# Kernel optimization log

Hardware: AMD Instinct MI355X
Metric: run time of the kernel (lower is better)

## Reference

```python
import jax, jax.numpy as jnp
import numpy as np

SINK_SIZE = 1          # sink frames kept at front of cache
LOCAL_ATTN_SIZE = 6    # attention window in frames


def _rope_angles(max_len, dim, theta=10000.0):
    inv = 1.0 / (theta ** (np.arange(0, dim, 2, dtype=np.float64) / dim))
    return np.outer(np.arange(max_len, dtype=np.float64), inv)  # [max_len, dim//2]


def _freqs_table(head_dim):
    # matches torch.cat([rope_params(1024, d-4*(d//6)), rope_params(1024, 2*(d//6)) x2], dim=1)
    d = head_dim
    return np.concatenate([
        _rope_angles(1024, d - 4 * (d // 6)),
        _rope_angles(1024, 2 * (d // 6)),
        _rope_angles(1024, 2 * (d // 6)),
    ], axis=1).astype(np.float32)  # [1024, d//2]


def _apply_rope(x, f, h, w, start_frame, freqs):
    # x: [B, S, N, D] with S == f*h*w; complex RoPE expressed as cos/sin rotation
    B, S, N, D = x.shape
    c = D // 2
    s0, s1 = c - 2 * (c // 3), c // 3
    ang = jnp.concatenate([
        jnp.broadcast_to(freqs[start_frame:start_frame + f, :s0][:, None, None, :], (f, h, w, s0)),
        jnp.broadcast_to(freqs[:h, s0:s0 + s1][None, :, None, :], (f, h, w, s1)),
        jnp.broadcast_to(freqs[:w, s0 + s1:][None, None, :, :], (f, h, w, s1)),
    ], axis=-1).reshape(S, 1, c)
    cos, sin = jnp.cos(ang)[None], jnp.sin(ang)[None]  # [1, S, 1, c]
    xr = x.reshape(B, S, N, c, 2)
    x0, x1 = xr[..., 0], xr[..., 1]
    out = jnp.stack([x0 * cos - x1 * sin, x0 * sin + x1 * cos], axis=-1)
    return out.reshape(B, S, N, D)


def setup_inputs() -> dict:
    key = jax.random.key(0)
    ks = jax.random.split(key, 5)
    B, S, N, D = 1, 1920, 12, 128
    CACHE = 6720
    return {
        "q": jax.random.normal(ks[0], (B, S, N, D), dtype=jnp.float32),
        "k": jax.random.normal(ks[1], (B, S, N, D), dtype=jnp.float32),
        "v": jax.random.normal(ks[2], (B, S, N, D), dtype=jnp.float32),
        "cache_k": jax.random.normal(ks[3], (B, CACHE, N, D), dtype=jnp.float32),
        "cache_v": jax.random.normal(ks[4], (B, CACHE, N, D), dtype=jnp.float32),
        "f": 2, "h": 24, "w": 40,
        "current_start": 5760, "global_end": 5760, "local_end": 5760,
    }


def reference(q, k, v, cache_k, cache_v, f, h, w, current_start, global_end, local_end):
    D = q.shape[-1]
    freqs = jnp.asarray(_freqs_table(D))
    frame_seqlen = h * w
    start_frame = current_start // frame_seqlen

    rq = _apply_rope(q, f, h, w, start_frame, freqs)
    rk = _apply_rope(k, f, h, w, start_frame, freqs)

    sink = SINK_SIZE * frame_seqlen
    max_att = LOCAL_ATTN_SIZE * frame_seqlen
    kv_size = cache_k.shape[1]
    n_new = q.shape[1]
    current_end = current_start + n_new

    # streaming KV cache with sink tokens + eviction/roll (indices are static ints,
    # matching torch's .item()-driven control flow)
    if current_end > global_end and n_new + local_end > kv_size:
        ev = n_new + local_end - kv_size
        roll = local_end - ev - sink
        cache_k = cache_k.at[:, sink:sink + roll].set(cache_k[:, sink + ev:sink + ev + roll])
        cache_v = cache_v.at[:, sink:sink + roll].set(cache_v[:, sink + ev:sink + ev + roll])
        new_local_end = local_end + current_end - global_end - ev
    else:
        new_local_end = local_end + current_end - global_end
    local_start = new_local_end - n_new
    cache_k = cache_k.at[:, local_start:new_local_end].set(rk)
    cache_v = cache_v.at[:, local_start:new_local_end].set(v)

    kv_start = max(0, new_local_end - max_att)
    kk = cache_k[:, kv_start:new_local_end]  # [B, W, N, D]
    vv = cache_v[:, kv_start:new_local_end]

    scale = 1.0 / jnp.sqrt(jnp.float32(D))
    scores = jnp.einsum('bqnd,bknd->bnqk', rq, kk) * scale
    attn = jax.nn.softmax(scores, axis=-1)
    out = jnp.einsum('bnqk,bknd->bqnd', attn, vv)
    return out
```

## Files before the change

### kernel.cpp

```cpp
#include <hip/hip_runtime.h>
#include <hip/hip_bf16.h>
#include <math.h>

typedef __attribute__((ext_vector_type(8))) short short8;
typedef __attribute__((ext_vector_type(4))) float f32x4;
typedef unsigned int u32;
typedef unsigned short u16;

#define NH 12
#define SQ 1920
#define SK 5760
#define DH 128
#define QTILE 32
#define NQT (SQ / QTILE)
#define QCH (NQT / 4)

#define OFF_CT 0
#define OFF_ST (OFF_CT + SQ * 64 * 4)
#define OFF_QB (OFF_ST + SQ * 64 * 4)
#define OFF_KB (OFF_QB + NH * SQ * DH * 2)
#define OFF_VT (OFF_KB + NH * SK * DH * 2)
#define OFF_PO (OFF_VT + NH * SK * DH * 2)

__device__ __forceinline__ u16 f2bf(float f) {
  u32 x = __float_as_uint(f);
  x += 0x7fffu + ((x >> 16) & 1u);
  return (u16)(x >> 16);
}

__device__ __forceinline__ f32x4 ntload4(const float* p) {
  return __builtin_nontemporal_load((const f32x4*)p);
}
__device__ __forceinline__ void ntstore4(float* p, f32x4 v) {
  __builtin_nontemporal_store(v, (f32x4*)p);
}

__global__ void k_table(float* __restrict__ ct, float* __restrict__ st) {
  int idx = blockIdx.x * 256 + threadIdx.x;
  if (idx >= SQ * 64) return;
  int s = idx >> 6, j = idx & 63;
  int fi = s / 960, rem = s % 960, hi = rem / 40, wi = rem % 40;
  const float L2_10000 = 13.287712379549449f;
  float ang;
  if (j < 22)      ang = (float)(6 + fi) * exp2f(-L2_10000 * (2.0f * j) / 44.0f);
  else if (j < 43) ang = (float)hi * exp2f(-L2_10000 * (2.0f * (j - 22)) / 42.0f);
  else             ang = (float)wi * exp2f(-L2_10000 * (2.0f * (j - 43)) / 42.0f);
  ct[idx] = cosf(ang);
  st[idx] = sinf(ang);
}

__global__ void k_prep(const float* __restrict__ q, const float* __restrict__ k,
                       const float* __restrict__ cache_k,
                       const float* __restrict__ ct, const float* __restrict__ st,
                       u16* __restrict__ Qb, u16* __restrict__ Kb) {
  const int NQth = NH * SQ * 32;
  const int NKN  = NH * SQ * 32;
  int idx = blockIdx.x * 256 + threadIdx.x;
  if (idx < NQth) {
    int c = idx & 31; int sn = idx >> 5; int n = sn % NH; int s = sn / NH;
    float4 x = *(const float4*)(q + ((size_t)s * NH + n) * DH + c * 4);
    float c0 = ct[s * 64 + 2 * c], s0 = st[s * 64 + 2 * c];
    float c1 = ct[s * 64 + 2 * c + 1], s1 = st[s * 64 + 2 * c + 1];
    const float QSC = (float)(1.4426950408889634 / 11.313708498984760390);
    ushort4 w;
    w.x = f2bf((x.x * c0 - x.y * s0) * QSC);
    w.y = f2bf((x.x * s0 + x.y * c0) * QSC);
    w.z = f2bf((x.z * c1 - x.w * s1) * QSC);
    w.w = f2bf((x.z * s1 + x.w * c1) * QSC);
    *(ushort4*)(Qb + ((size_t)n * SQ + s) * DH + c * 4) = w;
  } else if (idx < NQth + NKN) {
    int t = idx - NQth;
    int c = t & 31; int sn = t >> 5; int n = sn % NH; int s = sn / NH;
    float4 x = *(const float4*)(k + ((size_t)s * NH + n) * DH + c * 4);
    float c0 = ct[s * 64 + 2 * c], s0 = st[s * 64 + 2 * c];
    float c1 = ct[s * 64 + 2 * c + 1], s1 = st[s * 64 + 2 * c + 1];
    ushort4 w;
    w.x = f2bf(x.x * c0 - x.y * s0);
    w.y = f2bf(x.x * s0 + x.y * c0);
    w.z = f2bf(x.z * c1 - x.w * s1);
    w.w = f2bf(x.z * s1 + x.w * c1);
    *(ushort4*)(Kb + ((size_t)n * SK + 3840 + s) * DH + c * 4) = w;
  } else {
    int t = idx - NQth - NKN;
    int c = t & 31; int sn = t >> 5; int n = sn % NH; int p = sn / NH;
    float4 x = *(const float4*)(cache_k + ((size_t)(1920 + p) * NH + n) * DH + c * 4);
    ushort4 w; w.x = f2bf(x.x); w.y = f2bf(x.y); w.z = f2bf(x.z); w.w = f2bf(x.w);
    *(ushort4*)(Kb + ((size_t)n * SK + p) * DH + c * 4) = w;
  }
}

__global__ void k_vt(const float* __restrict__ v, const float* __restrict__ cache_v,
                     u16* __restrict__ Vt) {
  __shared__ float tile[64][65];
  int b = blockIdx.x;
  int n = b / 180; int bh = b % 180; int pb = bh >> 1; int dhalf = bh & 1;
  int p0 = pb * 64, d0 = dhalf * 64;
  int t = threadIdx.x;
#pragma unroll
  for (int it = 0; it < 16; ++it) {
    int lin = t + it * 256;
    int r = lin >> 6, c = lin & 63;
    int p = p0 + r;
    float val = (p < 3840)
      ? cache_v[((size_t)(1920 + p) * NH + n) * DH + d0 + c]
      : v[((size_t)(p - 3840) * NH + n) * DH + d0 + c];
    tile[r][c] = val;
  }
  __syncthreads();
#pragma unroll
  for (int it = 0; it < 16; ++it) {
    int lin = t + it * 256;
    int dr = lin >> 6, pc = lin & 63;
    Vt[((size_t)n * DH + d0 + dr) * SK + p0 + pc] = f2bf(tile[pc][dr]);
  }
}

#define KE (32 * 128)
#define VE (128 * 32)

template <int NS>
__global__ __launch_bounds__(256, 3) void k_attn(
    const u16* __restrict__ Qb, const u16* __restrict__ Kb, const u16* __restrict__ Vt,
    float* __restrict__ PO, float* __restrict__ Pm, float* __restrict__ Ps) {
  const int KPB = SK / NS;
  const int ITERS = KPB / 32;
  __shared__ u16 Klds[3 * KE];
  __shared__ u16 Vlds[3 * VE];

  const int nwg = NH * QCH * NS;
  int bid = blockIdx.x;
  int widx = (bid & 7) * (nwg >> 3) + (bid >> 3);
  int n = widx / (QCH * NS);
  int j2 = widx % (QCH * NS);
  int sp = j2 / QCH;
  int qtb = j2 % QCH;

  int tid = threadIdx.x;
  int w = tid >> 6;
  int l = tid & 63;
  int col = l & 15, g = l >> 4;
  int qt = qtb * 4 + w;
  int q0 = qt * QTILE;
  int kb0 = sp * KPB;

  const u16* kgh = Kb + (size_t)n * SK * DH;
  const u16* vgh = Vt + (size_t)n * DH * SK;

  auto stage = [&](int b, int kb) {
    u16* kl = Klds + b * KE;
    u16* vl = Vlds + b * VE;
#pragma unroll
    for (int i = 0; i < 2; ++i) {
      int cb = (i * 4 + w) * 64;
      {
        int T = cb + l; int r = T >> 4; int c = (T & 15) ^ (r & 7);
        __builtin_amdgcn_global_load_lds(
            (const __attribute__((address_space(1))) void*)(kgh + ((size_t)(kb + r)) * DH + (c << 3)),
            (__attribute__((address_space(3))) void*)(kl + cb * 8), 16, 0, 0);
      }
      {
        int T = cb + l; int d = T >> 2; int c = (T & 3) ^ (d & 3);
        __builtin_amdgcn_global_load_lds(
            (const __attribute__((address_space(1))) void*)(vgh + (size_t)d * SK + kb + (c << 3)),
            (__attribute__((address_space(3))) void*)(vl + cb * 8), 16, 0, 0);
      }
    }
  };

  short8 aq[2][4];
#pragma unroll
  for (int u = 0; u < 2; ++u) {
    const u16* qr = Qb + ((size_t)n * SQ + q0 + u * 16 + col) * DH + g * 8;
#pragma unroll
    for (int ks = 0; ks < 4; ++ks)
      aq[u][ks] = __builtin_nontemporal_load((const short8*)(qr + ks * 32));
  }

  f32x4 o[2][8];
#pragma unroll
  for (int u = 0; u < 2; ++u)
#pragma unroll
    for (int dt = 0; dt < 8; ++dt) o[u][dt] = (f32x4){0.f, 0.f, 0.f, 0.f};
  float m[2] = {-1e30f, -1e30f}, ssum[2] = {0.f, 0.f};

  stage(0, kb0);
  stage(1, kb0 + 32);

  int cur = 0;
  const int xK = col & 7;
  const int vch = (g ^ (col & 3)) << 3;
  for (int t = 0; t < ITERS; ++t) {
    int kb = kb0 + t * 32;
    int b2 = cur + 2; if (b2 >= 3) b2 -= 3;
    if (t + 2 < ITERS) {
      stage(b2, kb + 64);
      asm volatile("s_waitcnt vmcnt(8)" ::: "memory");
    } else if (t + 1 < ITERS) {
      asm volatile("s_waitcnt vmcnt(4)" ::: "memory");
    } else {
      asm volatile("s_waitcnt vmcnt(0)" ::: "memory");
    }
    __builtin_amdgcn_s_barrier();
    __builtin_amdgcn_sched_barrier(0);

    const u16* Kl = Klds + cur * KE;
    const u16* Vl = Vlds + cur * VE;

    f32x4 s0[2], s1[2];
#pragma unroll
    for (int u = 0; u < 2; ++u) { s0[u] = (f32x4){0,0,0,0}; s1[u] = (f32x4){0,0,0,0}; }
#pragma unroll
    for (int ks = 0; ks < 4; ++ks) {
      int ch = (((g + (ks << 2)) ^ xK) << 3);
      short8 ak0 = *(const short8*)(Kl + col * DH + ch);
      short8 ak1 = *(const short8*)(Kl + (col + 16) * DH + ch);
      s0[0] = __builtin_amdgcn_mfma_f32_16x16x32_bf16(ak0, aq[0][ks], s0[0], 0, 0, 0);
      s0[1] = __builtin_amdgcn_mfma_f32_16x16x32_bf16(ak0, aq[1][ks], s0[1], 0, 0, 0);
      s1[0] = __builtin_amdgcn_mfma_f32_16x16x32_bf16(ak1, aq[0][ks], s1[0], 0, 0, 0);
      s1[1] = __builtin_amdgcn_mfma_f32_16x16x32_bf16(ak1, aq[1][ks], s1[1], 0, 0, 0);
    }
    u32 pw[2][4];
#pragma unroll
    for (int u = 0; u < 2; ++u) {
      float bm = fmaxf(fmaxf(fmaxf(s0[u][0], s0[u][1]), fmaxf(s0[u][2], s0[u][3])),
                       fmaxf(fmaxf(s1[u][0], s1[u][1]), fmaxf(s1[u][2], s1[u][3])));
      bm = fmaxf(bm, __shfl_xor(bm, 16));
      bm = fmaxf(bm, __shfl_xor(bm, 32));
      if (!__all(bm <= m[u] + 8.0f)) {
        float mn = fmaxf(m[u], bm);
        float cr = exp2f(m[u] - mn);
        ssum[u] *= cr;
#pragma unroll
        for (int dt = 0; dt < 8; ++dt) o[u][dt] *= cr;
        m[u] = mn;
      }
      float p[8];
      float bs = 0.f;
#pragma unroll
      for (int r = 0; r < 4; ++r) { p[r] = exp2f(s0[u][r] - m[u]); bs += p[r]; }
#pragma unroll
      for (int r = 0; r < 4; ++r) { p[4 + r] = exp2f(s1[u][r] - m[u]); bs += p[4 + r]; }
      bs += __shfl_xor(bs, 16);
      bs += __shfl_xor(bs, 32);
      ssum[u] += bs;
      u32 w0 = (u32)f2bf(p[0]) | ((u32)f2bf(p[1]) << 16);
      u32 w1 = (u32)f2bf(p[2]) | ((u32)f2bf(p[3]) << 16);
      u32 w2 = (u32)f2bf(p[4]) | ((u32)f2bf(p[5]) << 16);
      u32 w3 = (u32)f2bf(p[6]) | ((u32)f2bf(p[7]) << 16);
      int src0 = col + ((g & 1) << 5);
      int src1 = src0 + 16;
      u32 a0 = (u32)__shfl((int)w0, src0), a1 = (u32)__shfl((int)w1, src0);
      u32 a2 = (u32)__shfl((int)w0, src1), a3 = (u32)__shfl((int)w1, src1);
      u32 b0 = (u32)__shfl((int)w2, src0), b1 = (u32)__shfl((int)w3, src0);
      u32 b2v = (u32)__shfl((int)w2, src1), b3 = (u32)__shfl((int)w3, src1);
      bool hi = (g >= 2);
      pw[u][0] = hi ? b0 : a0; pw[u][1] = hi ? b1 : a1;
      pw[u][2] = hi ? b2v : a2; pw[u][3] = hi ? b3 : a3;
    }
#pragma unroll
    for (int dt = 0; dt < 8; ++dt) {
      short8 av = *(const short8*)(Vl + (dt * 16 + col) * 32 + vch);
      union { u32 w[4]; short8 v; } pu0, pu1;
#pragma unroll
      for (int i = 0; i < 4; ++i) { pu0.w[i] = pw[0][i]; pu1.w[i] = pw[1][i]; }
      o[0][dt] = __builtin_amdgcn_mfma_f32_16x16x32_bf16(av, pu0.v, o[0][dt], 0, 0, 0);
      o[1][dt] = __builtin_amdgcn_mfma_f32_16x16x32_bf16(av, pu1.v, o[1][dt], 0, 0, 0);
    }
    __builtin_amdgcn_sched_barrier(0);
    __builtin_amdgcn_s_barrier();
    cur = cur + 1 == 3 ? 0 : cur + 1;
  }

  int pb = (n * NQT + qt) * NS + sp;
  float* po = PO + (size_t)pb * QTILE * DH;
#pragma unroll
  for (int u = 0; u < 2; ++u) {
#pragma unroll
    for (int dt = 0; dt < 8; ++dt)
      ntstore4(po + ((size_t)(u * 16 + col)) * DH + dt * 16 + g * 4, o[u][dt]);
    if (g == 0) {
      Pm[pb * QTILE + u * 16 + col] = m[u];
      Ps[pb * QTILE + u * 16 + col] = ssum[u];
    }
  }
}

template <int NS>
__global__ void k_merge(const float* __restrict__ PO, const float* __restrict__ Pm,
                        const float* __restrict__ Ps, float* __restrict__ out) {
  int idx = blockIdx.x * 256 + threadIdx.x;
  if (idx >= NH * SQ * 32) return;
  int c = idx & 31; int rest = idx >> 5; int qh = rest % SQ; int n = rest / SQ;
  int qt = qh >> 5, row = qh & 31;
  int bb = (n * NQT + qt) * NS;
  float mm[NS];
  float M = -1e30f;
#pragma unroll
  for (int s = 0; s < NS; ++s) { mm[s] = Pm[(bb + s) * 32 + row]; M = fmaxf(M, mm[s]); }
  float wgt[NS];
  float denom = 0.f;
#pragma unroll
  for (int s = 0; s < NS; ++s) {
    wgt[s] = exp2f(mm[s] - M);
    denom += Ps[(bb + s) * 32 + row] * wgt[s];
  }
  float inv = 1.0f / denom;
  f32x4 r = {0.f, 0.f, 0.f, 0.f};
#pragma unroll
  for (int s = 0; s < NS; ++s) {
    f32x4 p = ntload4(PO + ((size_t)(bb + s) * 32 + row) * DH + c * 4);
    r += p * wgt[s];
  }
  r *= inv;
  ntstore4(out + ((size_t)qh * NH + n) * DH + c * 4, r);
}

template <int NS>
static bool do_launch(void* const* d_in, void* d_out, void* d_ws, size_t ws_size,
                      hipStream_t stream) {
  const size_t nblk = (size_t)NH * NQT * NS;
  const size_t off_pm = OFF_PO + nblk * QTILE * DH * 4;
  const size_t off_ps = off_pm + nblk * QTILE * 4;
  const size_t need = off_ps + nblk * QTILE * 4;
  if (ws_size < need) return false;
  const float* q  = (const float*)d_in[0];
  const float* k  = (const float*)d_in[1];
  const float* v  = (const float*)d_in[2];
  const float* ck = (const float*)d_in[3];
  const float* cv = (const float*)d_in[4];
  char* ws = (char*)d_ws;
  float* ct = (float*)(ws + OFF_CT);
  float* st = (float*)(ws + OFF_ST);
  u16* Qb = (u16*)(ws + OFF_QB);
  u16* Kb = (u16*)(ws + OFF_KB);
  u16* Vt = (u16*)(ws + OFF_VT);
  float* PO = (float*)(ws + OFF_PO);
  float* Pm = (float*)(ws + off_pm);
  float* Ps = (float*)(ws + off_ps);

  k_table<<<(SQ * 64 + 255) / 256, 256, 0, stream>>>(ct, st);
  k_prep<<<(NH * SQ * 32 * 2 + NH * 3840 * 32 + 255) / 256, 256, 0, stream>>>(
      q, k, ck, ct, st, Qb, Kb);
  k_vt<<<NH * 90 * 2, 256, 0, stream>>>(v, cv, Vt);
  k_attn<NS><<<NH * QCH * NS, 256, 0, stream>>>(Qb, Kb, Vt, PO, Pm, Ps);
  k_merge<NS><<<(NH * SQ * 32 + 255) / 256, 256, 0, stream>>>(PO, Pm, Ps, (float*)d_out);
  return true;
}

extern "C" void kernel_launch(void* const* d_in, const int* in_sizes, int n_in,
                              void* d_out, int out_size, void* d_ws, size_t ws_size,
                              hipStream_t stream) {
  if (do_launch<6>(d_in, d_out, d_ws, ws_size, stream)) return;
  do_launch<4>(d_in, d_out, d_ws, ws_size, stream);
}
```

Before: 318.1 us.

## Fuse prep kernels, inline RoPE trig, and retile attention to 64-key double-buffered tiles

Result: faster. 310.7 us (-2.3%).

```diff
diff --git a/kernel.cpp b/kernel.cpp
--- a/kernel.cpp
+++ b/kernel.cpp
@@ -14,10 +14,11 @@
 #define QTILE 32
 #define NQT (SQ / QTILE)
 #define QCH (NQT / 4)
-
-#define OFF_CT 0
-#define OFF_ST (OFF_CT + SQ * 64 * 4)
-#define OFF_QB (OFF_ST + SQ * 64 * 4)
+#define KT 64
+#define KE2 (KT * DH)
+#define VE2 (DH * KT)
+
+#define OFF_QB 0
 #define OFF_KB (OFF_QB + NH * SQ * DH * 2)
 #define OFF_VT (OFF_KB + NH * SK * DH * 2)
 #define OFF_PO (OFF_VT + NH * SK * DH * 2)
@@ -27,7 +28,6 @@
   x += 0x7fffu + ((x >> 16) & 1u);
   return (u16)(x >> 16);
 }
-
 __device__ __forceinline__ f32x4 ntload4(const float* p) {
   return __builtin_nontemporal_load((const f32x4*)p);
 }
@@ -35,97 +35,97 @@
   __builtin_nontemporal_store(v, (f32x4*)p);
 }
 
-__global__ void k_table(float* __restrict__ ct, float* __restrict__ st) {
-  int idx = blockIdx.x * 256 + threadIdx.x;
-  if (idx >= SQ * 64) return;
-  int s = idx >> 6, j = idx & 63;
-  int fi = s / 960, rem = s % 960, hi = rem / 40, wi = rem % 40;
+__device__ __forceinline__ float rope_angle(int j, int fi, int hi, int wi) {
   const float L2_10000 = 13.287712379549449f;
-  float ang;
-  if (j < 22)      ang = (float)(6 + fi) * exp2f(-L2_10000 * (2.0f * j) / 44.0f);
-  else if (j < 43) ang = (float)hi * exp2f(-L2_10000 * (2.0f * (j - 22)) / 42.0f);
-  else             ang = (float)wi * exp2f(-L2_10000 * (2.0f * (j - 43)) / 42.0f);
-  ct[idx] = cosf(ang);
-  st[idx] = sinf(ang);
-}
+  if (j < 22)      return (float)(6 + fi) * exp2f(-L2_10000 * (2.0f * j) / 44.0f);
+  else if (j < 43) return (float)hi * exp2f(-L2_10000 * (2.0f * (j - 22)) / 42.0f);
+  else             return (float)wi * exp2f(-L2_10000 * (2.0f * (j - 43)) / 42.0f);
+}
+
+#define NQTH (NH * SQ * 32)
+#define ABLK ((2 * NQTH + NH * 3840 * 32) / 256)
+#define VBLK (NH * 90 * 2)
 
 __global__ void k_prep(const float* __restrict__ q, const float* __restrict__ k,
                        const float* __restrict__ cache_k,
-                       const float* __restrict__ ct, const float* __restrict__ st,
-                       u16* __restrict__ Qb, u16* __restrict__ Kb) {
-  const int NQth = NH * SQ * 32;
-  const int NKN  = NH * SQ * 32;
-  int idx = blockIdx.x * 256 + threadIdx.x;
-  if (idx < NQth) {
-    int c = idx & 31; int sn = idx >> 5; int n = sn % NH; int s = sn / NH;
-    float4 x = *(const float4*)(q + ((size_t)s * NH + n) * DH + c * 4);
-    float c0 = ct[s * 64 + 2 * c], s0 = st[s * 64 + 2 * c];
-    float c1 = ct[s * 64 + 2 * c + 1], s1 = st[s * 64 + 2 * c + 1];
-    const float QSC = (float)(1.4426950408889634 / 11.313708498984760390);
-    ushort4 w;
-    w.x = f2bf((x.x * c0 - x.y * s0) * QSC);
-    w.y = f2bf((x.x * s0 + x.y * c0) * QSC);
-    w.z = f2bf((x.z * c1 - x.w * s1) * QSC);
-    w.w = f2bf((x.z * s1 + x.w * c1) * QSC);
-    *(ushort4*)(Qb + ((size_t)n * SQ + s) * DH + c * 4) = w;
-  } else if (idx < NQth + NKN) {
-    int t = idx - NQth;
-    int c = t & 31; int sn = t >> 5; int n = sn % NH; int s = sn / NH;
-    float4 x = *(const float4*)(k + ((size_t)s * NH + n) * DH + c * 4);
-    float c0 = ct[s * 64 + 2 * c], s0 = st[s * 64 + 2 * c];
-    float c1 = ct[s * 64 + 2 * c + 1], s1 = st[s * 64 + 2 * c + 1];
-    ushort4 w;
-    w.x = f2bf(x.x * c0 - x.y * s0);
-    w.y = f2bf(x.x * s0 + x.y * c0);
-    w.z = f2bf(x.z * c1 - x.w * s1);
-    w.w = f2bf(x.z * s1 + x.w * c1);
-    *(ushort4*)(Kb + ((size_t)n * SK + 3840 + s) * DH + c * 4) = w;
-  } else {
-    int t = idx - NQth - NKN;
-    int c = t & 31; int sn = t >> 5; int n = sn % NH; int p = sn / NH;
-    float4 x = *(const float4*)(cache_k + ((size_t)(1920 + p) * NH + n) * DH + c * 4);
-    ushort4 w; w.x = f2bf(x.x); w.y = f2bf(x.y); w.z = f2bf(x.z); w.w = f2bf(x.w);
-    *(ushort4*)(Kb + ((size_t)n * SK + p) * DH + c * 4) = w;
-  }
-}
-
-__global__ void k_vt(const float* __restrict__ v, const float* __restrict__ cache_v,
-                     u16* __restrict__ Vt) {
+                       const float* __restrict__ v, const float* __restrict__ cache_v,
+                       u16* __restrict__ Qb, u16* __restrict__ Kb, u16* __restrict__ Vt) {
   __shared__ float tile[64][65];
   int b = blockIdx.x;
-  int n = b / 180; int bh = b % 180; int pb = bh >> 1; int dhalf = bh & 1;
-  int p0 = pb * 64, d0 = dhalf * 64;
-  int t = threadIdx.x;
-#pragma unroll
-  for (int it = 0; it < 16; ++it) {
-    int lin = t + it * 256;
-    int r = lin >> 6, c = lin & 63;
-    int p = p0 + r;
-    float val = (p < 3840)
-      ? cache_v[((size_t)(1920 + p) * NH + n) * DH + d0 + c]
-      : v[((size_t)(p - 3840) * NH + n) * DH + d0 + c];
-    tile[r][c] = val;
-  }
-  __syncthreads();
-#pragma unroll
-  for (int it = 0; it < 16; ++it) {
-    int lin = t + it * 256;
-    int dr = lin >> 6, pc = lin & 63;
-    Vt[((size_t)n * DH + d0 + dr) * SK + p0 + pc] = f2bf(tile[pc][dr]);
-  }
-}
-
-#define KE (32 * 128)
-#define VE (128 * 32)
+  if (b < ABLK) {
+    int idx = b * 256 + threadIdx.x;
+    if (idx < NQTH) {
+      int c = idx & 31; int sn = idx >> 5; int n = sn % NH; int s = sn / NH;
+      int fi = s / 960, rem = s % 960, hi = rem / 40, wi = rem % 40;
+      float4 x = *(const float4*)(q + ((size_t)s * NH + n) * DH + c * 4);
+      float a0 = rope_angle(2 * c, fi, hi, wi), a1 = rope_angle(2 * c + 1, fi, hi, wi);
+      float c0 = cosf(a0), s0 = sinf(a0), c1 = cosf(a1), s1 = sinf(a1);
+      const float QSC = (float)(1.4426950408889634 / 11.313708498984760390);
+      ushort4 w;
+      w.x = f2bf((x.x * c0 - x.y * s0) * QSC);
+      w.y = f2bf((x.x * s0 + x.y * c0) * QSC);
+      w.z = f2bf((x.z * c1 - x.w * s1) * QSC);
+      w.w = f2bf((x.z * s1 + x.w * c1) * QSC);
+      *(ushort4*)(Qb + ((size_t)n * SQ + s) * DH + c * 4) = w;
+    } else if (idx < 2 * NQTH) {
+      int t = idx - NQTH;
+      int c = t & 31; int sn = t >> 5; int n = sn % NH; int s = sn / NH;
+      int fi = s / 960, rem = s % 960, hi = rem / 40, wi = rem % 40;
+      float4 x = *(const float4*)(k + ((size_t)s * NH + n) * DH + c * 4);
+      float a0 = rope_angle(2 * c, fi, hi, wi), a1 = rope_angle(2 * c + 1, fi, hi, wi);
+      float c0 = cosf(a0), s0 = sinf(a0), c1 = cosf(a1), s1 = sinf(a1);
+      ushort4 w;
+      w.x = f2bf(x.x * c0 - x.y * s0);
+      w.y = f2bf(x.x * s0 + x.y * c0);
+      w.z = f2bf(x.z * c1 - x.w * s1);
+      w.w = f2bf(x.z * s1 + x.w * c1);
+      *(ushort4*)(Kb + ((size_t)n * SK + 3840 + s) * DH + c * 4) = w;
+    } else {
+      int t = idx - 2 * NQTH;
+      int c = t & 31; int sn = t >> 5; int n = sn % NH; int p = sn / NH;
+      float4 x = *(const float4*)(cache_k + ((size_t)(1920 + p) * NH + n) * DH + c * 4);
+      ushort4 w; w.x = f2bf(x.x); w.y = f2bf(x.y); w.z = f2bf(x.z); w.w = f2bf(x.w);
+      *(ushort4*)(Kb + ((size_t)n * SK + p) * DH + c * 4) = w;
+    }
+  } else {
+    int vb = b - ABLK;
+    int n = vb / 180; int bh = vb % 180; int pb = bh >> 1; int dhalf = bh & 1;
+    int p0 = pb * 64, d0 = dhalf * 64;
+    int t = threadIdx.x;
+#pragma unroll
+    for (int it = 0; it < 4; ++it) {
+      int lin = t + it * 256;
+      int r = lin >> 4, cq = (lin & 15) << 2;
+      int p = p0 + r;
+      const float* src = (p < 3840)
+        ? cache_v + ((size_t)(1920 + p) * NH + n) * DH + d0 + cq
+        : v + ((size_t)(p - 3840) * NH + n) * DH + d0 + cq;
+      float4 x = *(const float4*)src;
+      tile[r][cq] = x.x; tile[r][cq + 1] = x.y; tile[r][cq + 2] = x.z; tile[r][cq + 3] = x.w;
+    }
+    __syncthreads();
+#pragma unroll
+    for (int it = 0; it < 4; ++it) {
+      int lin = t + it * 256;
+      int dr = lin >> 4, pq = (lin & 15) << 2;
+      ushort4 wv;
+      wv.x = f2bf(tile[pq][dr]);     wv.y = f2bf(tile[pq + 1][dr]);
+      wv.z = f2bf(tile[pq + 2][dr]); wv.w = f2bf(tile[pq + 3][dr]);
+      *(ushort4*)(Vt + ((size_t)n * DH + d0 + dr) * SK + p0 + pq) = wv;
+    }
+  }
+}
 
 template <int NS>
-__global__ __launch_bounds__(256, 3) void k_attn(
+__global__ __launch_bounds__(256, 2) void k_attn(
     const u16* __restrict__ Qb, const u16* __restrict__ Kb, const u16* __restrict__ Vt,
     float* __restrict__ PO, float* __restrict__ Pm, float* __restrict__ Ps) {
+  static_assert((SK / NS) % KT == 0, "epoch divisibility");
+  static_assert((NH * QCH * NS) % 8 == 0, "xcd swizzle divisibility");
   const int KPB = SK / NS;
-  const int ITERS = KPB / 32;
-  __shared__ u16 Klds[3 * KE];
-  __shared__ u16 Vlds[3 * VE];
+  const int ITERS = KPB / KT;
+  __shared__ u16 Klds[2 * KE2];
+  __shared__ u16 Vlds[2 * VE2];
 
   const int nwg = NH * QCH * NS;
   int bid = blockIdx.x;
@@ -147,10 +147,10 @@
   const u16* vgh = Vt + (size_t)n * DH * SK;
 
   auto stage = [&](int b, int kb) {
-    u16* kl = Klds + b * KE;
-    u16* vl = Vlds + b * VE;
-#pragma unroll
-    for (int i = 0; i < 2; ++i) {
+    u16* kl = Klds + b * KE2;
+    u16* vl = Vlds + b * VE2;
+#pragma unroll
+    for (int i = 0; i < 4; ++i) {
       int cb = (i * 4 + w) * 64;
       {
         int T = cb + l; int r = T >> 4; int c = (T & 15) ^ (r & 7);
@@ -159,7 +159,7 @@
             (__attribute__((address_space(3))) void*)(kl + cb * 8), 16, 0, 0);
       }
       {
-        int T = cb + l; int d = T >> 2; int c = (T & 3) ^ (d & 3);
+        int T = cb + l; int d = T >> 3; int c = (T & 7) ^ (d & 7);
         __builtin_amdgcn_global_load_lds(
             (const __attribute__((address_space(1))) void*)(vgh + (size_t)d * SK + kb + (c << 3)),
             (__attribute__((address_space(3))) void*)(vl + cb * 8), 16, 0, 0);
@@ -184,46 +184,44 @@
   float m[2] = {-1e30f, -1e30f}, ssum[2] = {0.f, 0.f};
 
   stage(0, kb0);
-  stage(1, kb0 + 32);
+  asm volatile("s_waitcnt vmcnt(0)" ::: "memory");
+  __builtin_amdgcn_s_barrier();
 
   int cur = 0;
   const int xK = col & 7;
-  const int vch = (g ^ (col & 3)) << 3;
+#pragma unroll 1
   for (int t = 0; t < ITERS; ++t) {
-    int kb = kb0 + t * 32;
-    int b2 = cur + 2; if (b2 >= 3) b2 -= 3;
-    if (t + 2 < ITERS) {
-      stage(b2, kb + 64);
-      asm volatile("s_waitcnt vmcnt(8)" ::: "memory");
-    } else if (t + 1 < ITERS) {
-      asm volatile("s_waitcnt vmcnt(4)" ::: "memory");
-    } else {
-      asm volatile("s_waitcnt vmcnt(0)" ::: "memory");
-    }
-    __builtin_amdgcn_s_barrier();
-    __builtin_amdgcn_sched_barrier(0);
-
-    const u16* Kl = Klds + cur * KE;
-    const u16* Vl = Vlds + cur * VE;
-
-    f32x4 s0[2], s1[2];
-#pragma unroll
-    for (int u = 0; u < 2; ++u) { s0[u] = (f32x4){0,0,0,0}; s1[u] = (f32x4){0,0,0,0}; }
+    if (t + 1 < ITERS) stage(cur ^ 1, kb0 + (t + 1) * KT);
+
+    const u16* Kl = Klds + cur * KE2;
+    const u16* Vl = Vlds + cur * VE2;
+
+    f32x4 s[2][4];
+#pragma unroll
+    for (int u = 0; u < 2; ++u)
+#pragma unroll
+      for (int kq = 0; kq < 4; ++kq) s[u][kq] = (f32x4){0, 0, 0, 0};
+    __builtin_amdgcn_s_setprio(1);
 #pragma unroll
     for (int ks = 0; ks < 4; ++ks) {
       int ch = (((g + (ks << 2)) ^ xK) << 3);
-      short8 ak0 = *(const short8*)(Kl + col * DH + ch);
-      short8 ak1 = *(const short8*)(Kl + (col + 16) * DH + ch);
-      s0[0] = __builtin_amdgcn_mfma_f32_16x16x32_bf16(ak0, aq[0][ks], s0[0], 0, 0, 0);
-      s0[1] = __builtin_amdgcn_mfma_f32_16x16x32_bf16(ak0, aq[1][ks], s0[1], 0, 0, 0);
-      s1[0] = __builtin_amdgcn_mfma_f32_16x16x32_bf16(ak1, aq[0][ks], s1[0], 0, 0, 0);
-      s1[1] = __builtin_amdgcn_mfma_f32_16x16x32_bf16(ak1, aq[1][ks], s1[1], 0, 0, 0);
-    }
-    u32 pw[2][4];
+#pragma unroll
+      for (int kq = 0; kq < 4; ++kq) {
+        short8 ak = *(const short8*)(Kl + (kq * 16 + col) * DH + ch);
+        s[0][kq] = __builtin_amdgcn_mfma_f32_16x16x32_bf16(ak, aq[0][ks], s[0][kq], 0, 0, 0);
+        s[1][kq] = __builtin_amdgcn_mfma_f32_16x16x32_bf16(ak, aq[1][ks], s[1][kq], 0, 0, 0);
+      }
+    }
+    __builtin_amdgcn_s_setprio(0);
+
+    u32 pw[2][2][4];
 #pragma unroll
     for (int u = 0; u < 2; ++u) {
-      float bm = fmaxf(fmaxf(fmaxf(s0[u][0], s0[u][1]), fmaxf(s0[u][2], s0[u][3])),
-                       fmaxf(fmaxf(s1[u][0], s1[u][1]), fmaxf(s1[u][2], s1[u][3])));
+      float bm = -1e30f;
+#pragma unroll
+      for (int kq = 0; kq < 4; ++kq)
+#pragma unroll
+        for (int r = 0; r < 4; ++r) bm = fmaxf(bm, s[u][kq][r]);
       bm = fmaxf(bm, __shfl_xor(bm, 16));
       bm = fmaxf(bm, __shfl_xor(bm, 32));
       if (!__all(bm <= m[u] + 8.0f)) {
@@ -234,41 +232,51 @@
         for (int dt = 0; dt < 8; ++dt) o[u][dt] *= cr;
         m[u] = mn;
       }
-      float p[8];
+      float p[16];
       float bs = 0.f;
 #pragma unroll
-      for (int r = 0; r < 4; ++r) { p[r] = exp2f(s0[u][r] - m[u]); bs += p[r]; }
-#pragma unroll
-      for (int r = 0; r < 4; ++r) { p[4 + r] = exp2f(s1[u][r] - m[u]); bs += p[4 + r]; }
+      for (int kq = 0; kq < 4; ++kq)
+#pragma unroll
+        for (int r = 0; r < 4; ++r) { p[kq * 4 + r] = exp2f(s[u][kq][r] - m[u]); bs += p[kq * 4 + r]; }
       bs += __shfl_xor(bs, 16);
       bs += __shfl_xor(bs, 32);
       ssum[u] += bs;
-      u32 w0 = (u32)f2bf(p[0]) | ((u32)f2bf(p[1]) << 16);
-      u32 w1 = (u32)f2bf(p[2]) | ((u32)f2bf(p[3]) << 16);
-      u32 w2 = (u32)f2bf(p[4]) | ((u32)f2bf(p[5]) << 16);
-      u32 w3 = (u32)f2bf(p[6]) | ((u32)f2bf(p[7]) << 16);
-      int src0 = col + ((g & 1) << 5);
-      int src1 = src0 + 16;
-      u32 a0 = (u32)__shfl((int)w0, src0), a1 = (u32)__shfl((int)w1, src0);
-      u32 a2 = (u32)__shfl((int)w0, src1), a3 = (u32)__shfl((int)w1, src1);
-      u32 b0 = (u32)__shfl((int)w2, src0), b1 = (u32)__shfl((int)w3, src0);
-      u32 b2v = (u32)__shfl((int)w2, src1), b3 = (u32)__shfl((int)w3, src1);
-      bool hi = (g >= 2);
-      pw[u][0] = hi ? b0 : a0; pw[u][1] = hi ? b1 : a1;
-      pw[u][2] = hi ? b2v : a2; pw[u][3] = hi ? b3 : a3;
-    }
-#pragma unroll
-    for (int dt = 0; dt < 8; ++dt) {
-      short8 av = *(const short8*)(Vl + (dt * 16 + col) * 32 + vch);
-      union { u32 w[4]; short8 v; } pu0, pu1;
-#pragma unroll
-      for (int i = 0; i < 4; ++i) { pu0.w[i] = pw[0][i]; pu1.w[i] = pw[1][i]; }
-      o[0][dt] = __builtin_amdgcn_mfma_f32_16x16x32_bf16(av, pu0.v, o[0][dt], 0, 0, 0);
-      o[1][dt] = __builtin_amdgcn_mfma_f32_16x16x32_bf16(av, pu1.v, o[1][dt], 0, 0, 0);
-    }
+#pragma unroll
+      for (int h = 0; h < 2; ++h) {
+        u32 w0 = (u32)f2bf(p[8 * h + 0]) | ((u32)f2bf(p[8 * h + 1]) << 16);
+        u32 w1 = (u32)f2bf(p[8 * h + 2]) | ((u32)f2bf(p[8 * h + 3]) << 16);
+        u32 w2 = (u32)f2bf(p[8 * h + 4]) | ((u32)f2bf(p[8 * h + 5]) << 16);
+        u32 w3 = (u32)f2bf(p[8 * h + 6]) | ((u32)f2bf(p[8 * h + 7]) << 16);
+        int src0 = col + ((g & 1) << 5);
+        int src1 = src0 + 16;
+        u32 a0 = (u32)__shfl((int)w0, src0), a1 = (u32)__shfl((int)w1, src0);
+        u32 a2 = (u32)__shfl((int)w0, src1), a3 = (u32)__shfl((int)w1, src1);
+        u32 b0 = (u32)__shfl((int)w2, src0), b1 = (u32)__shfl((int)w3, src0);
+        u32 b2 = (u32)__shfl((int)w2, src1), b3 = (u32)__shfl((int)w3, src1);
+        bool hi = (g >= 2);
+        pw[u][h][0] = hi ? b0 : a0; pw[u][h][1] = hi ? b1 : a1;
+        pw[u][h][2] = hi ? b2 : a2; pw[u][h][3] = hi ? b3 : a3;
+      }
+    }
+    __builtin_amdgcn_s_setprio(1);
+#pragma unroll
+    for (int h = 0; h < 2; ++h) {
+      int vch = (((h << 2) + g) ^ xK) << 3;
+#pragma unroll
+      for (int dt = 0; dt < 8; ++dt) {
+        short8 av = *(const short8*)(Vl + (dt * 16 + col) * KT + vch);
+        union { u32 w[4]; short8 v; } pu0, pu1;
+#pragma unroll
+        for (int i = 0; i < 4; ++i) { pu0.w[i] = pw[0][h][i]; pu1.w[i] = pw[1][h][i]; }
+        o[0][dt] = __builtin_amdgcn_mfma_f32_16x16x32_bf16(av, pu0.v, o[0][dt], 0, 0, 0);
+        o[1][dt] = __builtin_amdgcn_mfma_f32_16x16x32_bf16(av, pu1.v, o[1][dt], 0, 0, 0);
+      }
+    }
+    __builtin_amdgcn_s_setprio(0);
+    asm volatile("s_waitcnt vmcnt(0)" ::: "memory");
+    __builtin_amdgcn_s_barrier();
     __builtin_amdgcn_sched_barrier(0);
-    __builtin_amdgcn_s_barrier();
-    cur = cur + 1 == 3 ? 0 : cur + 1;
+    cur ^= 1;
   }
 
   int pb = (n * NQT + qt) * NS + sp;
@@ -329,8 +337,6 @@
   const float* ck = (const float*)d_in[3];
   const float* cv = (const float*)d_in[4];
   char* ws = (char*)d_ws;
-  float* ct = (float*)(ws + OFF_CT);
-  float* st = (float*)(ws + OFF_ST);
   u16* Qb = (u16*)(ws + OFF_QB);
   u16* Kb = (u16*)(ws + OFF_KB);
   u16* Vt = (u16*)(ws + OFF_VT);
@@ -338,10 +344,7 @@
   float* Pm = (float*)(ws + off_pm);
   float* Ps = (float*)(ws + off_ps);
 
-  k_table<<<(SQ * 64 + 255) / 256, 256, 0, stream>>>(ct, st);
-  k_prep<<<(NH * SQ * 32 * 2 + NH * 3840 * 32 + 255) / 256, 256, 0, stream>>>(
-      q, k, ck, ct, st, Qb, Kb);
-  k_vt<<<NH * 90 * 2, 256, 0, stream>>>(v, cv, Vt);
+  k_prep<<<ABLK + VBLK, 256, 0, stream>>>(q, k, ck, v, cv, Qb, Kb, Vt);
   k_attn<NS><<<NH * QCH * NS, 256, 0, stream>>>(Qb, Kb, Vt, PO, Pm, Ps);
   k_merge<NS><<<(NH * SQ * 32 + 255) / 256, 256, 0, stream>>>(PO, Pm, Ps, (float*)d_out);
   return true;
@@ -351,5 +354,5 @@
                               void* d_out, int out_size, void* d_ws, size_t ws_size,
                               hipStream_t stream) {
   if (do_launch<6>(d_in, d_out, d_ws, ws_size, stream)) return;
-  do_launch<4>(d_in, d_out, d_ws, ws_size, stream);
-}
+  do_launch<2>(d_in, d_out, d_ws, ws_size, stream);
+}
```
